# Optimization experiments

Measured on AMD Instinct MI355X. Metric: run time of the kernel, lower is better.

The kernel has to match this reference:

```python
import jax, jax.numpy as jnp
import numpy as np

B, T, V, E, H = 256, 512, 30000, 256, 32


def _run_dir(x, mask, Wih, Whh, bih, bhh, reverse):
    # x: [B,T,D], mask: [B,T] bool. PyTorch GRU gate order: r, z, n.
    gi = jnp.einsum('btd,gd->btg', x, Wih) + bih  # precompute input gates [B,T,3H]
    h0 = jnp.zeros((x.shape[0], Whh.shape[1]), x.dtype)

    def step(h, inp):
        gi_t, m_t = inp
        gh = h @ Whh.T + bhh
        ir, iz, inn = jnp.split(gi_t, 3, axis=-1)
        hr, hz, hn = jnp.split(gh, 3, axis=-1)
        r = jax.nn.sigmoid(ir + hr)
        z = jax.nn.sigmoid(iz + hz)
        n = jnp.tanh(inn + r * hn)
        h_new = (1.0 - z) * n + z * h
        # packed-sequence semantics: freeze state at padded steps
        h = jnp.where(m_t[:, None], h_new, h)
        return h, h

    hT, ys = jax.lax.scan(step, h0, (jnp.swapaxes(gi, 0, 1), mask.T), reverse=reverse)
    return jnp.swapaxes(ys, 0, 1), hT  # outputs [B,T,H], final hidden [B,H]


def _bigru_layer(x, mask, pf, pb):
    of, hf = _run_dir(x, mask, *pf, reverse=False)
    ob, hb = _run_dir(x, mask, *pb, reverse=True)
    return jnp.concatenate([of, ob], axis=-1), hf, hb


def setup_inputs() -> dict:
    key = jax.random.key(0)
    ks = jax.random.split(key, 24)
    lengths = jax.random.randint(ks[0], (B,), 1, T + 1)
    mask = (jnp.arange(T)[None, :] < lengths[:, None]).astype(jnp.int32)
    ids = jax.random.randint(ks[1], (B, T), 1, V)
    ids = jnp.where(mask > 0, ids, 0)  # pad_id = 0 at padded positions
    embed = (jax.random.normal(ks[2], (V, E), jnp.float32) * 0.1).at[0].set(0.0)

    def gru_params(k, din):
        k1, k2, k3, k4 = jax.random.split(k, 4)
        s = 1.0 / np.sqrt(H)
        return (jax.random.uniform(k1, (3 * H, din), jnp.float32, -s, s),
                jax.random.uniform(k2, (3 * H, H), jnp.float32, -s, s),
                jax.random.uniform(k3, (3 * H,), jnp.float32, -s, s),
                jax.random.uniform(k4, (3 * H,), jnp.float32, -s, s))

    inp = {"input_ids": ids, "attention_mask": mask, "embed": embed}
    i = 3
    for layer, din in (("l0", E), ("l1", 2 * H)):
        for d in ("f", "b"):
            Wih, Whh, bih, bhh = gru_params(ks[i], din); i += 1
            inp[f"Wih_{layer}{d}"] = Wih
            inp[f"Whh_{layer}{d}"] = Whh
            inp[f"bih_{layer}{d}"] = bih
            inp[f"bhh_{layer}{d}"] = bhh
    s = 1.0 / np.sqrt(2 * H)
    inp["Wout"] = jax.random.uniform(ks[i], (6, 2 * H), jnp.float32, -s, s)
    inp["bout"] = jax.random.uniform(ks[i + 1], (6,), jnp.float32, -s, s)
    return inp


def reference(input_ids, attention_mask, embed,
              Wih_l0f, Whh_l0f, bih_l0f, bhh_l0f,
              Wih_l0b, Whh_l0b, bih_l0b, bhh_l0b,
              Wih_l1f, Whh_l1f, bih_l1f, bhh_l1f,
              Wih_l1b, Whh_l1b, bih_l1b, bhh_l1b,
              Wout, bout):
    mask = attention_mask > 0
    x = embed[input_ids]  # [B,T,E]
    x1, _, _ = _bigru_layer(x, mask,
                            (Wih_l0f, Whh_l0f, bih_l0f, bhh_l0f),
                            (Wih_l0b, Whh_l0b, bih_l0b, bhh_l0b))
    # no dropout: eval-mode forward
    _, hf, hb = _bigru_layer(x1, mask,
                             (Wih_l1f, Whh_l1f, bih_l1f, bhh_l1f),
                             (Wih_l1b, Whh_l1b, bih_l1b, bhh_l1b))
    top = jnp.concatenate([hf, hb], axis=-1)  # h_n[-2:] -> [B, 2H]
    return top @ Wout.T + bout  # [B, 6]
```

## Files before the change

### kernel.cpp

```cpp
#include <hip/hip_runtime.h>
#include <hip/hip_bf16.h>
#include <stdint.h>

#define B_ 256
#define T_ 512
#define V_ 30000
#define E_ 256
#define H_ 32

typedef float v2f __attribute__((ext_vector_type(2)));

#define LOG2E_F 1.44269504088896340736f

__device__ __forceinline__ float exp2_fast(float x) {
    float r; asm("v_exp_f32 %0, %1" : "=v"(r) : "v"(x)); return r;
}
__device__ __forceinline__ float rcp_fast(float x) {
    float r; asm("v_rcp_f32 %0, %1" : "=v"(r) : "v"(x)); return r;
}
__device__ __forceinline__ void pk_fma(v2f& acc, v2f w, v2f h) {
    asm("v_pk_fma_f32 %0, %1, %2, %0" : "+v"(acc) : "v"(w), "v"(h));
}
template <int CTRL>
__device__ __forceinline__ float mdpp(float x) {
    return __int_as_float(
        __builtin_amdgcn_mov_dpp(__float_as_int(x), CTRL, 0xF, 0xF, true));
}
#define DPP_XOR1  0xB1
#define DPP_XOR2  0x4E
#define DPP_XOR3  0x1B
#define DPP_XOR7  0x141
#define DPP_XOR15 0x140

#define GEMM_MT 64
#define GEMM_KC 32
#define GEMM_PA 68
#define GEMM_PB 196

__global__ __launch_bounds__(256) void gemm_gates(
    const float* __restrict__ A, int M, int K,
    const float* __restrict__ Wf, const float* __restrict__ Wb,
    const float* __restrict__ bihf, const float* __restrict__ bhhf,
    const float* __restrict__ bihb, const float* __restrict__ bhhb,
    float* __restrict__ Out)
{
    __shared__ float As[GEMM_KC][GEMM_PA];
    __shared__ float Bs[GEMM_KC][GEMM_PB];

    const int tid = threadIdx.x;
    const int mbase = blockIdx.x * GEMM_MT;
    const int mg = tid >> 5, ng = tid & 31;
    const int m_off = mg * 8, n_off = ng * 6;

    float acc[8][6];
    #pragma unroll
    for (int r = 0; r < 8; ++r)
        #pragma unroll
        for (int c = 0; c < 6; ++c) acc[r][c] = 0.f;

    for (int kc = 0; kc < K; kc += GEMM_KC) {
        #pragma unroll
        for (int i = 0; i < 2; ++i) {
            int fi = tid + 256 * i;
            int row = fi >> 3, cf = fi & 7;
            int m = mbase + row;
            float4 v = make_float4(0.f, 0.f, 0.f, 0.f);
            if (m < M) v = *(const float4*)&A[(size_t)m * K + kc + cf * 4];
            As[cf * 4 + 0][row] = v.x; As[cf * 4 + 1][row] = v.y;
            As[cf * 4 + 2][row] = v.z; As[cf * 4 + 3][row] = v.w;
        }
        #pragma unroll
        for (int i = 0; i < 6; ++i) {
            int fi = tid + 256 * i;
            int g = fi >> 3, cf = fi & 7;
            const float* Wsel = (g < 96) ? (Wf + (size_t)g * K)
                                         : (Wb + (size_t)(g - 96) * K);
            float4 v = *(const float4*)&Wsel[kc + cf * 4];
            Bs[cf * 4 + 0][g] = v.x; Bs[cf * 4 + 1][g] = v.y;
            Bs[cf * 4 + 2][g] = v.z; Bs[cf * 4 + 3][g] = v.w;
        }
        __syncthreads();
        #pragma unroll
        for (int k = 0; k < GEMM_KC; ++k) {
            float a[8], bb[6];
            *(float4*)&a[0] = *(const float4*)&As[k][m_off];
            *(float4*)&a[4] = *(const float4*)&As[k][m_off + 4];
            *(float2*)&bb[0] = *(const float2*)&Bs[k][n_off];
            *(float2*)&bb[2] = *(const float2*)&Bs[k][n_off + 2];
            *(float2*)&bb[4] = *(const float2*)&Bs[k][n_off + 4];
            #pragma unroll
            for (int r = 0; r < 8; ++r)
                #pragma unroll
                for (int c = 0; c < 6; ++c)
                    acc[r][c] = fmaf(a[r], bb[c], acc[r][c]);
        }
        __syncthreads();
    }

    float bias[6], gsc[6];
    #pragma unroll
    for (int c = 0; c < 6; ++c) {
        int g = n_off + c;
        int g96 = (g < 96) ? g : g - 96;
        const float* bih = (g < 96) ? bihf : bihb;
        const float* bhh = (g < 96) ? bhhf : bhhb;
        bias[c] = bih[g96] + ((g96 < 64) ? bhh[g96] : 0.f);
        gsc[c]  = (g96 < 64) ? -LOG2E_F : 2.0f * LOG2E_F;
    }
    #pragma unroll
    for (int r = 0; r < 8; ++r) {
        int m = mbase + m_off + r;
        if (m < M) {
            float* op = &Out[(size_t)m * 192 + n_off];
            #pragma unroll
            for (int c = 0; c < 6; ++c) op[c] = (acc[r][c] + bias[c]) * gsc[c];
        }
    }
}

template <int USE_IDS>
__global__ __launch_bounds__(64, 1) void gru_scan(
    const float* __restrict__ gi,
    const int* __restrict__ ids,
    const int* __restrict__ mask,
    const float* __restrict__ Whh_f, const float* __restrict__ Whh_b,
    const float* __restrict__ bhh_f, const float* __restrict__ bhh_b,
    float* __restrict__ out_seq,
    float* __restrict__ out_fin)
{
    __shared__ float hsh[64];

    const int l = threadIdx.x;
    const int i16 = l & 15;
    const int rp = (l >> 4) & 1;
    const int j = l & 31;
    const bool lower = l < 32;
    const int dir = blockIdx.x & 1;
    const int b = blockIdx.x >> 1;
    const int bT = b * T_;

    const float* Whh = dir ? Whh_b : Whh_f;
    const float* bhh = dir ? bhh_b : bhh_f;

    const int kA = 16 * rp;
    const int kB = 16 - kA;

    const float sRZ = -LOG2E_F;
    const float sN2 = 2.0f * LOG2E_F;

    const int M0[8] = {0, 2, 7, 5, 15, 13, 8, 10};
    const int M1[8] = {1, 3, 6, 4, 14, 12, 9, 11};

    v2f wAR[8], wAZ[8], wAN[8], wBR[8], wBZ[8], wBN[8];
    #pragma unroll
    for (int q = 0; q < 8; ++q) {
        const int ka0 = kA + (i16 ^ M0[q]);
        const int ka1 = kA + (i16 ^ M1[q]);
        wAR[q] = (v2f){Whh[j * 32 + ka0] * sRZ, Whh[j * 32 + ka1] * sRZ};
        wAZ[q] = (v2f){Whh[(32 + j) * 32 + ka0] * sRZ,
                       Whh[(32 + j) * 32 + ka1] * sRZ};
        wAN[q] = (v2f){Whh[(64 + j) * 32 + ka0] * sN2,
                       Whh[(64 + j) * 32 + ka1] * sN2};
        v2f br = *(const v2f*)&Whh[j * 32 + kB + 2 * q];
        v2f bz = *(const v2f*)&Whh[(32 + j) * 32 + kB + 2 * q];
        v2f bn_ = *(const v2f*)&Whh[(64 + j) * 32 + kB + 2 * q];
        wBR[q] = (v2f){br.x * sRZ, br.y * sRZ};
        wBZ[q] = (v2f){bz.x * sRZ, bz.y * sRZ};
        wBN[q] = (v2f){bn_.x * sN2, bn_.y * sN2};
    }
    const float bns = bhh[64 + j] * sN2;

    const int offR = dir * 96 + j;
    const int offZ = dir * 96 + 32 + j;
    const int offN = dir * 96 + 64 + j;

    auto wbase = [&](int c) { return dir ? (bT + 508 - 4 * c) : (bT + 4 * c); };

    int4 ids0 = make_int4(0, 0, 0, 0);
    if (USE_IDS) ids0 = *(const int4*)&ids[wbase(0)];
    int4 mask_use = *(const int4*)&mask[wbase(0)];
    int4 mask_mid = *(const int4*)&mask[wbase(1)];
    int4 mask_in  = make_int4(0, 0, 0, 0);
    int4 ids_pf = make_int4(0, 0, 0, 0), ids_mid = ids_pf, ids_in = ids_pf;
    if (USE_IDS) {
        ids_pf  = *(const int4*)&ids[wbase(1)];
        ids_mid = *(const int4*)&ids[wbase(2)];
    }

    float gR[2][4], gZ[2][4], gN[2][4];
    #pragma unroll
    for (int u = 0; u < 4; ++u) {
        int row;
        if (USE_IDS) {
            const int* ip = (const int*)&ids0;
            row = dir ? ip[3 - u] : ip[u];
        } else {
            row = bT + (dir ? (511 - u) : u);
        }
        const float* gp = gi + (size_t)row * 192;
        gR[0][u] = gp[offR];
        gZ[0][u] = gp[offZ];
        gN[0][u] = gp[offN];
    }

    float h = 0.f;
    hsh[l] = 0.f;

    for (int c2 = 0; c2 < 64; ++c2) {
        #pragma unroll
        for (int pb = 0; pb < 2; ++pb) {
            const int c = 2 * c2 + pb;
            if (USE_IDS) {
                const int ci = (c + 3 < 128) ? (c + 3) : 127;
                ids_in = *(const int4*)&ids[wbase(ci)];
            }
            {
                const int cm = (c + 2 < 128) ? (c + 2) : 127;
                mask_in = *(const int4*)&mask[wbase(cm)];
            }
            const int cN = (c + 1 < 128) ? (c + 1) : 127;

            #pragma unroll
            for (int u = 0; u < 4; ++u) {
                int rowN;
                if (USE_IDS) {
                    const int* ip = (const int*)&ids_pf;
                    rowN = dir ? ip[3 - u] : ip[u];
                } else {
                    rowN = bT + (dir ? (511 - 4 * cN - u) : (4 * cN + u));
                }
                const float* gpN = gi + (size_t)rowN * 192;
                gR[pb ^ 1][u] = gpN[offR];
                gZ[pb ^ 1][u] = gpN[offZ];
                gN[pb ^ 1][u] = gpN[offN];

                const int* mu = (const int*)&mask_use;
                const int m = dir ? mu[3 - u] : mu[u];

                float4 o0 = *(const float4*)&hsh[kB + 0];
                float4 o1 = *(const float4*)&hsh[kB + 4];
                float4 o2 = *(const float4*)&hsh[kB + 8];
                float4 o3 = *(const float4*)&hsh[kB + 12];

                v2f p[8];
                p[0].x = h;                      p[0].y = mdpp<DPP_XOR1>(h);
                p[1].x = mdpp<DPP_XOR2>(h);      p[1].y = mdpp<DPP_XOR3>(h);
                p[2].x = mdpp<DPP_XOR7>(h);      p[2].y = mdpp<DPP_XOR7>(p[0].y);
                p[3].x = mdpp<DPP_XOR7>(p[1].x); p[3].y = mdpp<DPP_XOR7>(p[1].y);
                p[4].x = mdpp<DPP_XOR15>(h);     p[4].y = mdpp<DPP_XOR15>(p[0].y);
                p[5].x = mdpp<DPP_XOR15>(p[1].x); p[5].y = mdpp<DPP_XOR15>(p[1].y);
                p[6].x = mdpp<DPP_XOR15>(p[2].x); p[6].y = mdpp<DPP_XOR15>(p[2].y);
                p[7].x = mdpp<DPP_XOR15>(p[3].x); p[7].y = mdpp<DPP_XOR15>(p[3].y);

                v2f aAR = {0.f, 0.f}, aAZ = {0.f, 0.f}, aAN = {0.f, 0.f};
                #pragma unroll
                for (int q = 0; q < 8; ++q) {
                    pk_fma(aAR, wAR[q], p[q]);
                    pk_fma(aAZ, wAZ[q], p[q]);
                    pk_fma(aAN, wAN[q], p[q]);
                }

                v2f hB[8];
                hB[0] = (v2f){o0.x, o0.y}; hB[1] = (v2f){o0.z, o0.w};
                hB[2] = (v2f){o1.x, o1.y}; hB[3] = (v2f){o1.z, o1.w};
                hB[4] = (v2f){o2.x, o2.y}; hB[5] = (v2f){o2.z, o2.w};
                hB[6] = (v2f){o3.x, o3.y}; hB[7] = (v2f){o3.z, o3.w};

                v2f aB0R = {0.f, 0.f}, aB0Z = {0.f, 0.f}, aB0N = {0.f, 0.f};
                v2f aB1R = {0.f, 0.f}, aB1Z = {0.f, 0.f}, aB1N = {0.f, 0.f};
                #pragma unroll
                for (int q = 0; q < 4; ++q) {
                    pk_fma(aB0R, wBR[q], hB[q]);
                    pk_fma(aB0Z, wBZ[q], hB[q]);
                    pk_fma(aB0N, wBN[q], hB[q]);
                }
                #pragma unroll
                for (int q = 4; q < 8; ++q) {
                    pk_fma(aB1R, wBR[q], hB[q]);
                    pk_fma(aB1Z, wBZ[q], hB[q]);
                    pk_fma(aB1N, wBN[q], hB[q]);
                }

                const float yr = (gR[pb][u] + (aAR.x + aAR.y)) +
                                 ((aB0R.x + aB0R.y) + (aB1R.x + aB1R.y));
                const float yz = (gZ[pb][u] + (aAZ.x + aAZ.y)) +
                                 ((aB0Z.x + aB0Z.y) + (aB1Z.x + aB1Z.y));
                const float hns = (bns + (aAN.x + aAN.y)) +
                                  ((aB0N.x + aB0N.y) + (aB1N.x + aB1N.y));
                const float r = rcp_fast(1.0f + exp2_fast(yr));
                const float z = rcp_fast(1.0f + exp2_fast(yz));
                const float yn = gN[pb][u] + r * hns;
                const float n = fmaf(-2.0f, rcp_fast(1.0f + exp2_fast(yn)), 1.0f);
                const float hnew = n + z * (h - n);
                h = m ? hnew : h;

                hsh[l] = h;

                if (out_seq != nullptr) {
                    const int t = dir ? (511 - 4 * c - u) : (4 * c + u);
                    if (lower)
                        out_seq[(size_t)(bT + t) * 64 + dir * 32 + j] = h;
                }
            }
            mask_use = mask_mid; mask_mid = mask_in;
            if (USE_IDS) { ids_pf = ids_mid; ids_mid = ids_in; }
        }
    }

    if (out_fin != nullptr && lower)
        out_fin[b * 64 + dir * 32 + j] = h;
}

__global__ void head_kernel(const float* __restrict__ hfin,
                            const float* __restrict__ Wout,
                            const float* __restrict__ bout,
                            float* __restrict__ out)
{
    int idx = blockIdx.x * blockDim.x + threadIdx.x;
    if (idx >= B_ * 6) return;
    int b = idx / 6, o = idx % 6;
    float acc = bout[o];
    const float* hp = hfin + b * 64;
    const float* wp = Wout + o * 64;
    #pragma unroll
    for (int k = 0; k < 64; ++k) acc = fmaf(hp[k], wp[k], acc);
    out[idx] = acc;
}

extern "C" void kernel_launch(void* const* d_in, const int* in_sizes, int n_in,
                              void* d_out, int out_size, void* d_ws, size_t ws_size,
                              hipStream_t stream)
{
    const int*   ids   = (const int*)d_in[0];
    const int*   mask  = (const int*)d_in[1];
    const float* embed = (const float*)d_in[2];
    const float* Wih0f = (const float*)d_in[3];
    const float* Whh0f = (const float*)d_in[4];
    const float* bih0f = (const float*)d_in[5];
    const float* bhh0f = (const float*)d_in[6];
    const float* Wih0b = (const float*)d_in[7];
    const float* Whh0b = (const float*)d_in[8];
    const float* bih0b = (const float*)d_in[9];
    const float* bhh0b = (const float*)d_in[10];
    const float* Wih1f = (const float*)d_in[11];
    const float* Whh1f = (const float*)d_in[12];
    const float* bih1f = (const float*)d_in[13];
    const float* bhh1f = (const float*)d_in[14];
    const float* Wih1b = (const float*)d_in[15];
    const float* Whh1b = (const float*)d_in[16];
    const float* bih1b = (const float*)d_in[17];
    const float* bhh1b = (const float*)d_in[18];
    const float* Wout  = (const float*)d_in[19];
    const float* bout  = (const float*)d_in[20];

    float* ws   = (float*)d_ws;
    float* gbuf = ws;
    float* x1   = ws + (size_t)B_ * T_ * 192;
    float* hfin = x1 + (size_t)B_ * T_ * 64;

    gemm_gates<<<(V_ + GEMM_MT - 1) / GEMM_MT, 256, 0, stream>>>(
        embed, V_, E_, Wih0f, Wih0b, bih0f, bhh0f, bih0b, bhh0b, gbuf);

    gru_scan<1><<<2 * B_, 64, 0, stream>>>(
        gbuf, ids, mask, Whh0f, Whh0b, bhh0f, bhh0b, x1, nullptr);

    gemm_gates<<<(B_ * T_) / GEMM_MT, 256, 0, stream>>>(
        x1, B_ * T_, 64, Wih1f, Wih1b, bih1f, bhh1f, bih1b, bhh1b, gbuf);

    gru_scan<0><<<2 * B_, 64, 0, stream>>>(
        gbuf, nullptr, mask, Whh1f, Whh1b, bhh1f, bhh1b, nullptr, hfin);

    head_kernel<<<(B_ * 6 + 255) / 256, 256, 0, stream>>>(hfin, Wout, bout,
                                                          (float*)d_out);
}
```

Measured before the change: 528.4 us.

## Replace LDS hidden-state exchange with permlane32 swap and DPP in GRU scan

The recurrent scan no longer writes the hidden state to shared memory and reads the other half back each step. Instead it uses a permlane32 swap so each lane gets the opposite 32-lane half's value, then builds the permuted operands with DPP moves. Lanes are remapped so both half-wave rows hold matching hidden indices, and the B-half weights are loaded with the same XOR permutation. This takes LDS write/read latency and its wait off the serial dependency chain, at the cost of an extra DPP tree and register-pinning asm barriers.

```diff
diff --git a/kernel.cpp b/kernel.cpp
--- a/kernel.cpp
+++ b/kernel.cpp
@@ -9,6 +9,7 @@
 #define H_ 32
 
 typedef float v2f __attribute__((ext_vector_type(2)));
+typedef unsigned int uint2e __attribute__((ext_vector_type(2)));
 
 #define LOG2E_F 1.44269504088896340736f
 
@@ -31,6 +32,12 @@
 #define DPP_XOR3  0x1B
 #define DPP_XOR7  0x141
 #define DPP_XOR15 0x140
+
+__device__ __forceinline__ float swap32(float h) {
+    uint2e r = __builtin_amdgcn_permlane32_swap(
+        __float_as_uint(h), __float_as_uint(h), false, false);
+    return __uint_as_float(r.x ^ r.y ^ __float_as_uint(h));
+}
 
 #define GEMM_MT 64
 #define GEMM_KC 32
@@ -128,12 +135,11 @@
     float* __restrict__ out_seq,
     float* __restrict__ out_fin)
 {
-    __shared__ float hsh[64];
-
     const int l = threadIdx.x;
     const int i16 = l & 15;
-    const int rp = (l >> 4) & 1;
-    const int j = l & 31;
+    const int row = l >> 4;
+    const int hi = (row ^ (row >> 1)) & 1;
+    const int j = i16 + 16 * hi;
     const bool lower = l < 32;
     const int dir = blockIdx.x & 1;
     const int b = blockIdx.x >> 1;
@@ -142,7 +148,7 @@
     const float* Whh = dir ? Whh_b : Whh_f;
     const float* bhh = dir ? bhh_b : bhh_f;
 
-    const int kA = 16 * rp;
+    const int kA = 16 * hi;
     const int kB = 16 - kA;
 
     const float sRZ = -LOG2E_F;
@@ -154,21 +160,25 @@
     v2f wAR[8], wAZ[8], wAN[8], wBR[8], wBZ[8], wBN[8];
     #pragma unroll
     for (int q = 0; q < 8; ++q) {
-        const int ka0 = kA + (i16 ^ M0[q]);
-        const int ka1 = kA + (i16 ^ M1[q]);
-        wAR[q] = (v2f){Whh[j * 32 + ka0] * sRZ, Whh[j * 32 + ka1] * sRZ};
-        wAZ[q] = (v2f){Whh[(32 + j) * 32 + ka0] * sRZ,
-                       Whh[(32 + j) * 32 + ka1] * sRZ};
-        wAN[q] = (v2f){Whh[(64 + j) * 32 + ka0] * sN2,
-                       Whh[(64 + j) * 32 + ka1] * sN2};
-        v2f br = *(const v2f*)&Whh[j * 32 + kB + 2 * q];
-        v2f bz = *(const v2f*)&Whh[(32 + j) * 32 + kB + 2 * q];
-        v2f bn_ = *(const v2f*)&Whh[(64 + j) * 32 + kB + 2 * q];
-        wBR[q] = (v2f){br.x * sRZ, br.y * sRZ};
-        wBZ[q] = (v2f){bz.x * sRZ, bz.y * sRZ};
-        wBN[q] = (v2f){bn_.x * sN2, bn_.y * sN2};
-    }
-    const float bns = bhh[64 + j] * sN2;
+        const int a0 = kA + (i16 ^ M0[q]);
+        const int a1 = kA + (i16 ^ M1[q]);
+        const int b0 = kB + (i16 ^ M0[q]);
+        const int b1 = kB + (i16 ^ M1[q]);
+        wAR[q] = (v2f){Whh[j * 32 + a0] * sRZ, Whh[j * 32 + a1] * sRZ};
+        wAZ[q] = (v2f){Whh[(32 + j) * 32 + a0] * sRZ, Whh[(32 + j) * 32 + a1] * sRZ};
+        wAN[q] = (v2f){Whh[(64 + j) * 32 + a0] * sN2, Whh[(64 + j) * 32 + a1] * sN2};
+        wBR[q] = (v2f){Whh[j * 32 + b0] * sRZ, Whh[j * 32 + b1] * sRZ};
+        wBZ[q] = (v2f){Whh[(32 + j) * 32 + b0] * sRZ, Whh[(32 + j) * 32 + b1] * sRZ};
+        wBN[q] = (v2f){Whh[(64 + j) * 32 + b0] * sN2, Whh[(64 + j) * 32 + b1] * sN2};
+    }
+    float bns = bhh[64 + j] * sN2;
+
+    #pragma unroll
+    for (int q = 0; q < 8; ++q) {
+        asm volatile("" : "+v"(wAR[q]), "+v"(wAZ[q]), "+v"(wAN[q]),
+                          "+v"(wBR[q]), "+v"(wBZ[q]), "+v"(wBN[q]));
+    }
+    asm volatile("" : "+v"(bns));
 
     const int offR = dir * 96 + j;
     const int offZ = dir * 96 + 32 + j;
@@ -190,21 +200,20 @@
     float gR[2][4], gZ[2][4], gN[2][4];
     #pragma unroll
     for (int u = 0; u < 4; ++u) {
-        int row;
+        int rowi;
         if (USE_IDS) {
             const int* ip = (const int*)&ids0;
-            row = dir ? ip[3 - u] : ip[u];
+            rowi = dir ? ip[3 - u] : ip[u];
         } else {
-            row = bT + (dir ? (511 - u) : u);
-        }
-        const float* gp = gi + (size_t)row * 192;
+            rowi = bT + (dir ? (511 - u) : u);
+        }
+        const float* gp = gi + (size_t)rowi * 192;
         gR[0][u] = gp[offR];
         gZ[0][u] = gp[offZ];
         gN[0][u] = gp[offN];
     }
 
     float h = 0.f;
-    hsh[l] = 0.f;
 
     for (int c2 = 0; c2 < 64; ++c2) {
         #pragma unroll
@@ -237,64 +246,53 @@
                 const int* mu = (const int*)&mask_use;
                 const int m = dir ? mu[3 - u] : mu[u];
 
-                float4 o0 = *(const float4*)&hsh[kB + 0];
-                float4 o1 = *(const float4*)&hsh[kB + 4];
-                float4 o2 = *(const float4*)&hsh[kB + 8];
-                float4 o3 = *(const float4*)&hsh[kB + 12];
-
-                v2f p[8];
-                p[0].x = h;                      p[0].y = mdpp<DPP_XOR1>(h);
-                p[1].x = mdpp<DPP_XOR2>(h);      p[1].y = mdpp<DPP_XOR3>(h);
-                p[2].x = mdpp<DPP_XOR7>(h);      p[2].y = mdpp<DPP_XOR7>(p[0].y);
-                p[3].x = mdpp<DPP_XOR7>(p[1].x); p[3].y = mdpp<DPP_XOR7>(p[1].y);
-                p[4].x = mdpp<DPP_XOR15>(h);     p[4].y = mdpp<DPP_XOR15>(p[0].y);
-                p[5].x = mdpp<DPP_XOR15>(p[1].x); p[5].y = mdpp<DPP_XOR15>(p[1].y);
-                p[6].x = mdpp<DPP_XOR15>(p[2].x); p[6].y = mdpp<DPP_XOR15>(p[2].y);
-                p[7].x = mdpp<DPP_XOR15>(p[3].x); p[7].y = mdpp<DPP_XOR15>(p[3].y);
-
-                v2f aAR = {0.f, 0.f}, aAZ = {0.f, 0.f}, aAN = {0.f, 0.f};
+                const float hs = swap32(h);
+
+                v2f p[8], p2[8];
+                {
+                    p[0].x = h;                       p[0].y = mdpp<DPP_XOR1>(h);
+                    p[1].x = mdpp<DPP_XOR2>(h);       p[1].y = mdpp<DPP_XOR3>(h);
+                    p[2].x = mdpp<DPP_XOR7>(h);       p[2].y = mdpp<DPP_XOR7>(p[0].y);
+                    p[3].x = mdpp<DPP_XOR7>(p[1].x);  p[3].y = mdpp<DPP_XOR7>(p[1].y);
+                    p[4].x = mdpp<DPP_XOR15>(h);      p[4].y = mdpp<DPP_XOR15>(p[0].y);
+                    p[5].x = mdpp<DPP_XOR15>(p[1].x); p[5].y = mdpp<DPP_XOR15>(p[1].y);
+                    p[6].x = mdpp<DPP_XOR15>(p[2].x); p[6].y = mdpp<DPP_XOR15>(p[2].y);
+                    p[7].x = mdpp<DPP_XOR15>(p[3].x); p[7].y = mdpp<DPP_XOR15>(p[3].y);
+
+                    p2[0].x = hs;                       p2[0].y = mdpp<DPP_XOR1>(hs);
+                    p2[1].x = mdpp<DPP_XOR2>(hs);       p2[1].y = mdpp<DPP_XOR3>(hs);
+                    p2[2].x = mdpp<DPP_XOR7>(hs);       p2[2].y = mdpp<DPP_XOR7>(p2[0].y);
+                    p2[3].x = mdpp<DPP_XOR7>(p2[1].x);  p2[3].y = mdpp<DPP_XOR7>(p2[1].y);
+                    p2[4].x = mdpp<DPP_XOR15>(hs);      p2[4].y = mdpp<DPP_XOR15>(p2[0].y);
+                    p2[5].x = mdpp<DPP_XOR15>(p2[1].x); p2[5].y = mdpp<DPP_XOR15>(p2[1].y);
+                    p2[6].x = mdpp<DPP_XOR15>(p2[2].x); p2[6].y = mdpp<DPP_XOR15>(p2[2].y);
+                    p2[7].x = mdpp<DPP_XOR15>(p2[3].x); p2[7].y = mdpp<DPP_XOR15>(p2[3].y);
+                }
+
+                v2f aR0 = {0.f, 0.f}, aZ0 = {0.f, 0.f}, aN0 = {0.f, 0.f};
+                v2f aR1 = {0.f, 0.f}, aZ1 = {0.f, 0.f}, aN1 = {0.f, 0.f};
                 #pragma unroll
                 for (int q = 0; q < 8; ++q) {
-                    pk_fma(aAR, wAR[q], p[q]);
-                    pk_fma(aAZ, wAZ[q], p[q]);
-                    pk_fma(aAN, wAN[q], p[q]);
+                    pk_fma(aR0, wAR[q], p[q]);
+                    pk_fma(aZ0, wAZ[q], p[q]);
+                    pk_fma(aN0, wAN[q], p[q]);
+                    pk_fma(aR1, wBR[q], p2[q]);
+                    pk_fma(aZ1, wBZ[q], p2[q]);
+                    pk_fma(aN1, wBN[q], p2[q]);
                 }
-
-                v2f hB[8];
-                hB[0] = (v2f){o0.x, o0.y}; hB[1] = (v2f){o0.z, o0.w};
-                hB[2] = (v2f){o1.x, o1.y}; hB[3] = (v2f){o1.z, o1.w};
-                hB[4] = (v2f){o2.x, o2.y}; hB[5] = (v2f){o2.z, o2.w};
-                hB[6] = (v2f){o3.x, o3.y}; hB[7] = (v2f){o3.z, o3.w};
-
-                v2f aB0R = {0.f, 0.f}, aB0Z = {0.f, 0.f}, aB0N = {0.f, 0.f};
-                v2f aB1R = {0.f, 0.f}, aB1Z = {0.f, 0.f}, aB1N = {0.f, 0.f};
-                #pragma unroll
-                for (int q = 0; q < 4; ++q) {
-                    pk_fma(aB0R, wBR[q], hB[q]);
-                    pk_fma(aB0Z, wBZ[q], hB[q]);
-                    pk_fma(aB0N, wBN[q], hB[q]);
-                }
-                #pragma unroll
-                for (int q = 4; q < 8; ++q) {
-                    pk_fma(aB1R, wBR[q], hB[q]);
-                    pk_fma(aB1Z, wBZ[q], hB[q]);
-                    pk_fma(aB1N, wBN[q], hB[q]);
-                }
-
-                const float yr = (gR[pb][u] + (aAR.x + aAR.y)) +
-                                 ((aB0R.x + aB0R.y) + (aB1R.x + aB1R.y));
-                const float yz = (gZ[pb][u] + (aAZ.x + aAZ.y)) +
-                                 ((aB0Z.x + aB0Z.y) + (aB1Z.x + aB1Z.y));
-                const float hns = (bns + (aAN.x + aAN.y)) +
-                                  ((aB0N.x + aB0N.y) + (aB1N.x + aB1N.y));
+                const v2f sR = aR0 + aR1;
+                const v2f sZ = aZ0 + aZ1;
+                const v2f sN = aN0 + aN1;
+
+                const float yr  = (gR[pb][u] + sR.x) + sR.y;
+                const float yz  = (gZ[pb][u] + sZ.x) + sZ.y;
+                const float hns = (bns + sN.x) + sN.y;
                 const float r = rcp_fast(1.0f + exp2_fast(yr));
                 const float z = rcp_fast(1.0f + exp2_fast(yz));
                 const float yn = gN[pb][u] + r * hns;
                 const float n = fmaf(-2.0f, rcp_fast(1.0f + exp2_fast(yn)), 1.0f);
                 const float hnew = n + z * (h - n);
                 h = m ? hnew : h;
-
-                hsh[l] = h;
 
                 if (out_seq != nullptr) {
                     const int t = dir ? (511 - 4 * c - u) : (4 * c + u);
```

Result: no change. 525.4 us (-0.6%).
